# Kernel tuning notes

Hardware: AMD Instinct MI355X
Metric: run time of the kernel (lower is better)

The kernel has to match this reference:

```python
import jax, jax.numpy as jnp
import numpy as np

N, E, IN, HID, HEADS, EDGE_DIM, L = 50000, 800000, 128, 64, 4, 8, 2
NEG_SLOPE = 0.2


def setup_inputs() -> dict:
    key = jax.random.key(0)
    ks = jax.random.split(key, 12)
    s = 0.05
    return {
        "x": jax.random.normal(ks[0], (N, IN), jnp.float32),
        "edge_index": jax.random.randint(ks[1], (2, E), 0, N, jnp.int32),
        "edge_attr": jax.random.randint(ks[2], (E,), 0, 3, jnp.int32),
        "proj_w": jax.random.normal(ks[3], (IN, HID), jnp.float32) * s,
        "proj_b": jnp.zeros((HID,), jnp.float32),
        "edge_emb": jax.random.normal(ks[4], (3, EDGE_DIM), jnp.float32) * s,
        "Wl": jax.random.normal(ks[5], (L, HID, HEADS * HID), jnp.float32) * s,
        "Wr": jax.random.normal(ks[6], (L, HID, HEADS * HID), jnp.float32) * s,
        "We": jax.random.normal(ks[7], (L, EDGE_DIM, HEADS * HID), jnp.float32) * s,
        "att": jax.random.normal(ks[8], (L, HEADS, HID), jnp.float32) * s,
        "bias": jnp.zeros((L, HID), jnp.float32),
        "ln_w": jnp.ones((L, HID), jnp.float32),
        "ln_b": jnp.zeros((L, HID), jnp.float32),
    }


def _layer_norm(h, w, b, eps=1e-5):
    mu = h.mean(-1, keepdims=True)
    var = ((h - mu) ** 2).mean(-1, keepdims=True)
    return (h - mu) * jax.lax.rsqrt(var + eps) * w + b


def reference(x, edge_index, edge_attr, proj_w, proj_b, edge_emb, Wl, Wr, We, att, bias, ln_w, ln_b):
    n = x.shape[0]
    x = x @ proj_w + proj_b  # [N, HID]
    ef = edge_emb[edge_attr]  # [E, EDGE_DIM]
    # PyG GATv2Conv default: add self-loops, edge feature fill_value='mean'
    loop = jnp.arange(n, dtype=edge_index.dtype)
    src = jnp.concatenate([edge_index[0], loop])
    dst = jnp.concatenate([edge_index[1], loop])
    ef = jnp.concatenate([ef, jnp.broadcast_to(ef.mean(0), (n, ef.shape[1]))])  # [E+N, EDGE_DIM]

    for l in range(L):
        xl = (x @ Wl[l]).reshape(n, HEADS, HID)   # source transform
        xr = (x @ Wr[l]).reshape(n, HEADS, HID)   # target transform
        ee = (ef @ We[l]).reshape(-1, HEADS, HID)  # edge transform [E+N,H,C]
        m = xl[src] + xr[dst] + ee                # gather by edge -> [E+N,H,C]
        s = jnp.einsum('ehc,hc->eh', jax.nn.leaky_relu(m, NEG_SLOPE), att[l])
        # segment softmax over incoming edges of each dst node
        smax = jax.ops.segment_max(s, dst, num_segments=n)
        a = jnp.exp(s - smax[dst])
        denom = jax.ops.segment_sum(a, dst, num_segments=n)
        alpha = a / denom[dst]                    # [E+N, H]
        out = jax.ops.segment_sum(alpha[:, :, None] * xl[src], dst, num_segments=n)  # [N,H,C]
        out = out.mean(axis=1) + bias[l]          # concat=False -> head mean
        x = _layer_norm(out + x, ln_w[l], ln_b[l])
    return x
```

## Files before the change

### kernel.cpp

```cpp
#include <hip/hip_runtime.h>

constexpr int N_NODES = 50000;
constexpr int E_EDGES = 800000;
constexpr int SLOTS   = 64;
constexpr int IN_DIM  = 128;
constexpr int HID     = 64;
constexpr int HEADS   = 4;
constexpr int HH      = HEADS * HID;
constexpr int EDGE_DIM = 8;
constexpr int L_LAYERS = 2;
constexpr float NEG_SLOPE = 0.2f;
constexpr int N_STRIPS = N_NODES / 16;
constexpr int SCAT_BLKS = (E_EDGES + 255) / 256;
constexpr int PROJ_BLKS = (N_STRIPS + 15) / 16;
constexpr int CNT_BLKS  = 256;
constexpr int PAD_BLKS  = (N_NODES + 255) / 256;

typedef float floatx2 __attribute__((ext_vector_type(2)));
typedef float f32x4 __attribute__((ext_vector_type(4)));
typedef short bf16x8 __attribute__((ext_vector_type(8)));

__device__ __forceinline__ unsigned short f2bf(float f) {
    unsigned int b = __float_as_uint(f);
    unsigned int r = (b + 0x7FFFu + ((b >> 16) & 1u)) >> 16;
    return (unsigned short)r;
}
__device__ __forceinline__ float bf2f(unsigned short u) {
    return __uint_as_float(((unsigned int)u) << 16);
}
__device__ __forceinline__ float lrelu(float x) { return fmaxf(x, NEG_SLOPE * x); }

__device__ __forceinline__ unsigned char f2fp8(float v) {
    return (unsigned char)(__builtin_amdgcn_cvt_pk_fp8_f32(v, v, 0, false) & 0xFF);
}
__device__ __forceinline__ void fp8x4_to_f32(unsigned int w, float& a, float& b,
                                             float& c, float& d) {
    floatx2 lo = __builtin_amdgcn_cvt_pk_f32_fp8((int)w, false);
    floatx2 hi = __builtin_amdgcn_cvt_pk_f32_fp8((int)w, true);
    a = lo.x; b = lo.y; c = hi.x; d = hi.y;
}

__global__ void mega_kernel(const int* __restrict__ src, const int* __restrict__ dst,
                            const int* __restrict__ attr, int* __restrict__ cnt,
                            unsigned int* __restrict__ fcsr, int* __restrict__ counts,
                            const float* __restrict__ x, const float* __restrict__ w,
                            const float* __restrict__ b, float* __restrict__ x0) {
    __shared__ unsigned short wS[IN_DIM * HID];
    int bid = blockIdx.x;
    if (bid < SCAT_BLKS) {
        int e = bid * 256 + threadIdx.x;
        if (e >= E_EDGES) return;
        int d = dst[e];
        int pos = atomicAdd(&cnt[d], 1);
        if (pos < SLOTS - 1)
            fcsr[((size_t)d << 6) + pos] = (unsigned int)src[e] | ((unsigned int)attr[e] << 16);
        return;
    }
    bid -= SCAT_BLKS;
    if (bid < PROJ_BLKS) {
        for (int i = threadIdx.x; i < IN_DIM * HID; i += 256) wS[i] = f2bf(w[i]);
        __syncthreads();
        int wid = threadIdx.x >> 6, lane = threadIdx.x & 63;
        int colb = lane & 15, kb = (lane >> 4) * 8;
        bf16x8 bfr[4][4];
#pragma unroll
        for (int c = 0; c < 4; ++c)
#pragma unroll
            for (int g = 0; g < 4; ++g) {
                bf16x8 v;
#pragma unroll
                for (int j = 0; j < 8; ++j)
                    v[j] = (short)wS[(g * 32 + kb + j) * HID + c * 16 + colb];
                bfr[c][g] = v;
            }
        float bias_v[4];
#pragma unroll
        for (int c = 0; c < 4; ++c) bias_v[c] = b[c * 16 + colb];
#pragma unroll
        for (int i = 0; i < 4; ++i) {
            int s = bid * 16 + i * 4 + wid;
            if (s >= N_STRIPS) break;
            int row = s * 16 + colb;
            const float* xp = x + (size_t)row * IN_DIM + kb;
            bf16x8 af[4];
#pragma unroll
            for (int g = 0; g < 4; ++g) {
                float4 lo = *(const float4*)(xp + g * 32);
                float4 hi = *(const float4*)(xp + g * 32 + 4);
                bf16x8 v;
                v[0] = (short)f2bf(lo.x); v[1] = (short)f2bf(lo.y);
                v[2] = (short)f2bf(lo.z); v[3] = (short)f2bf(lo.w);
                v[4] = (short)f2bf(hi.x); v[5] = (short)f2bf(hi.y);
                v[6] = (short)f2bf(hi.z); v[7] = (short)f2bf(hi.w);
                af[g] = v;
            }
            int rbase = s * 16 + (lane >> 4) * 4;
#pragma unroll
            for (int c = 0; c < 4; ++c) {
                f32x4 acc = {0.f, 0.f, 0.f, 0.f};
#pragma unroll
                for (int g = 0; g < 4; ++g)
                    acc = __builtin_amdgcn_mfma_f32_16x16x32_bf16(af[g], bfr[c][g], acc, 0, 0, 0);
#pragma unroll
                for (int r = 0; r < 4; ++r)
                    x0[(size_t)(rbase + r) * HID + c * 16 + colb] = acc[r] + bias_v[c];
            }
        }
        return;
    }
    bid -= PROJ_BLKS;
    {
        int c0 = 0, c1 = 0, c2 = 0;
        for (int i = bid * 256 + threadIdx.x; i < E_EDGES; i += CNT_BLKS * 256) {
            int a = attr[i];
            c0 += (a == 0); c1 += (a == 1); c2 += (a == 2);
        }
        for (int o = 32; o; o >>= 1) {
            c0 += __shfl_down(c0, o);
            c1 += __shfl_down(c1, o);
            c2 += __shfl_down(c2, o);
        }
        if ((threadIdx.x & 63) == 0) {
            atomicAdd(&counts[0], c0);
            atomicAdd(&counts[1], c1);
            atomicAdd(&counts[2], c2);
        }
    }
}

__global__ void pad_eet_kernel(int* __restrict__ cnt, unsigned int* __restrict__ fcsr,
                               const float* __restrict__ edge_emb, const float* __restrict__ We,
                               const int* __restrict__ counts, float* __restrict__ eet) {
    if (blockIdx.x >= (unsigned)PAD_BLKS) {
        int hc = threadIdx.x;
        float inv = 1.f / (float)E_EDGES;
        for (int l = 0; l < L_LAYERS; ++l) {
            const float* We_l = We + (size_t)l * EDGE_DIM * HH;
            float* eet_l = eet + (size_t)l * 4 * HH;
            for (int t = 0; t < 3; ++t) {
                float acc = 0.f;
#pragma unroll
                for (int d = 0; d < EDGE_DIM; ++d) acc += edge_emb[t * EDGE_DIM + d] * We_l[d * HH + hc];
                eet_l[t * HH + hc] = acc;
            }
            float acc = 0.f;
#pragma unroll
            for (int d = 0; d < EDGE_DIM; ++d) {
                float md = (counts[0] * edge_emb[0 * EDGE_DIM + d] +
                            counts[1] * edge_emb[1 * EDGE_DIM + d] +
                            counts[2] * edge_emb[2 * EDGE_DIM + d]) * inv;
                acc += md * We_l[d * HH + hc];
            }
            eet_l[3 * HH + hc] = acc;
        }
        return;
    }
    int n = blockIdx.x * 256 + threadIdx.x;
    if (n >= N_NODES) return;
    int c = cnt[n];
    int tot = c + 1;
    int pad = (tot + 3) & ~3;
    unsigned int selfe = (unsigned int)n | (3u << 16);
    unsigned int* row = fcsr + ((size_t)n << 6);
    for (int p = c; p < pad; ++p) row[p] = selfe;
    cnt[n] = tot;
}

__global__ __launch_bounds__(256)
void transform_mfma_kernel(const float* __restrict__ x, const float* __restrict__ Wl,
                           const float* __restrict__ Wr, unsigned char* __restrict__ xl,
                           unsigned short* __restrict__ xr) {
    __shared__ unsigned short wS[HID * 512];
    for (int i = threadIdx.x; i < HID * 512; i += 256) {
        int k = i >> 9, c = i & 511;
        float v = (c < 256) ? Wl[k * 256 + c] : Wr[k * 256 + (c - 256)];
        wS[i] = f2bf(v);
    }
    __syncthreads();
    int wid = threadIdx.x >> 6, lane = threadIdx.x & 63;
    int colb = lane & 15, kb = (lane >> 4) * 8;
    bf16x8 bfr[8][2];
#pragma unroll
    for (int c = 0; c < 8; ++c)
#pragma unroll
        for (int g = 0; g < 2; ++g) {
            bf16x8 v;
            int col = wid * 128 + c * 16 + colb;
#pragma unroll
            for (int j = 0; j < 8; ++j)
                v[j] = (short)wS[(g * 32 + kb + j) * 512 + col];
            bfr[c][g] = v;
        }

    for (int i = 0; i < 16; ++i) {
        int s = blockIdx.x * 16 + i;
        if (s >= N_STRIPS) break;
        int row = s * 16 + colb;
        const float* xp = x + (size_t)row * HID + kb;
        bf16x8 af[2];
#pragma unroll
        for (int g = 0; g < 2; ++g) {
            float4 lo = *(const float4*)(xp + g * 32);
            float4 hi = *(const float4*)(xp + g * 32 + 4);
            bf16x8 v;
            v[0] = (short)f2bf(lo.x); v[1] = (short)f2bf(lo.y);
            v[2] = (short)f2bf(lo.z); v[3] = (short)f2bf(lo.w);
            v[4] = (short)f2bf(hi.x); v[5] = (short)f2bf(hi.y);
            v[6] = (short)f2bf(hi.z); v[7] = (short)f2bf(hi.w);
            af[g] = v;
        }
        int rbase = s * 16 + (lane >> 4) * 4;
#pragma unroll
        for (int c = 0; c < 8; ++c) {
            f32x4 acc = {0.f, 0.f, 0.f, 0.f};
            acc = __builtin_amdgcn_mfma_f32_16x16x32_bf16(af[0], bfr[c][0], acc, 0, 0, 0);
            acc = __builtin_amdgcn_mfma_f32_16x16x32_bf16(af[1], bfr[c][1], acc, 0, 0, 0);
            int col = wid * 128 + c * 16 + colb;
            if (col < 256) {
#pragma unroll
                for (int r = 0; r < 4; ++r)
                    xl[(size_t)(rbase + r) * HH + col] = f2fp8(acc[r]);
            } else {
                int c2 = col - 256;
#pragma unroll
                for (int r = 0; r < 4; ++r)
                    xr[(size_t)(rbase + r) * HH + c2] = f2bf(acc[r]);
            }
        }
    }
}

__global__ void gat_fused_kernel(const unsigned int* __restrict__ fcsr,
                                 const int* __restrict__ cnt,
                                 const unsigned char* __restrict__ xl,
                                 const unsigned short* __restrict__ xr,
                                 const float* __restrict__ eet_l, const float* __restrict__ att_l,
                                 const float* __restrict__ bias_l, const float* __restrict__ lnw,
                                 const float* __restrict__ lnb, const float* __restrict__ x_res,
                                 float* __restrict__ x_out) {
    __shared__ float4 eetS[256];
    eetS[threadIdx.x] = ((const float4*)eet_l)[threadIdx.x];
    __syncthreads();
    int n = blockIdx.x * 4 + (threadIdx.x >> 6);
    int lane = threadIdx.x & 63;
    float4 av = *(const float4*)(att_l + lane * 4);
    ushort4 xrv = *(const ushort4*)(xr + (size_t)n * HH + lane * 4);
    float xr0 = bf2f(xrv.x), xr1 = bf2f(xrv.y), xr2 = bf2f(xrv.z), xr3 = bf2f(xrv.w);
    const unsigned char* xlb = xl + lane * 4;
    int cntn = cnt[n];
    const unsigned int* cp = fcsr + ((size_t)n << 6);
    float accA0 = 0.f, accA1 = 0.f, accA2 = 0.f, accA3 = 0.f, denA = 0.f;
    float accB0 = 0.f, accB1 = 0.f, accB2 = 0.f, accB3 = 0.f, denB = 0.f;

    auto gat_round = [&](uint4 ew, unsigned int xw0, unsigned int xw1, unsigned int xw2,
                         unsigned int xw3, int rem) {
        int t0 = ew.x >> 16, t1 = ew.y >> 16, t2 = ew.z >> 16, t3 = ew.w >> 16;
        float4 ee0 = eetS[(t0 << 6) + lane];
        float4 ee1 = eetS[(t1 << 6) + lane];
        float4 ee2 = eetS[(t2 << 6) + lane];
        float4 ee3 = eetS[(t3 << 6) + lane];
        float a0, a1, a2, a3, b0, b1, b2, b3, c0, c1, c2, c3, d0, d1, d2, d3;
        fp8x4_to_f32(xw0, a0, a1, a2, a3);
        fp8x4_to_f32(xw1, b0, b1, b2, b3);
        fp8x4_to_f32(xw2, c0, c1, c2, c3);
        fp8x4_to_f32(xw3, d0, d1, d2, d3);
        float p0 = lrelu(a0 + xr0 + ee0.x) * av.x + lrelu(a1 + xr1 + ee0.y) * av.y +
                   lrelu(a2 + xr2 + ee0.z) * av.z + lrelu(a3 + xr3 + ee0.w) * av.w;
        float p1 = lrelu(b0 + xr0 + ee1.x) * av.x + lrelu(b1 + xr1 + ee1.y) * av.y +
                   lrelu(b2 + xr2 + ee1.z) * av.z + lrelu(b3 + xr3 + ee1.w) * av.w;
        float p2 = lrelu(c0 + xr0 + ee2.x) * av.x + lrelu(c1 + xr1 + ee2.y) * av.y +
                   lrelu(c2 + xr2 + ee2.z) * av.z + lrelu(c3 + xr3 + ee2.w) * av.w;
        float p3 = lrelu(d0 + xr0 + ee3.x) * av.x + lrelu(d1 + xr1 + ee3.y) * av.y +
                   lrelu(d2 + xr2 + ee3.z) * av.z + lrelu(d3 + xr3 + ee3.w) * av.w;
        p0 += __shfl_xor(p0, 1); p1 += __shfl_xor(p1, 1);
        p2 += __shfl_xor(p2, 1); p3 += __shfl_xor(p3, 1);
        p0 += __shfl_xor(p0, 2); p1 += __shfl_xor(p1, 2);
        p2 += __shfl_xor(p2, 2); p3 += __shfl_xor(p3, 2);
        p0 += __shfl_xor(p0, 4); p1 += __shfl_xor(p1, 4);
        p2 += __shfl_xor(p2, 4); p3 += __shfl_xor(p3, 4);
        p0 += __shfl_xor(p0, 8); p1 += __shfl_xor(p1, 8);
        p2 += __shfl_xor(p2, 8); p3 += __shfl_xor(p3, 8);
        float w0 = __expf(p0);
        float w1 = (rem > 1) ? __expf(p1) : 0.f;
        float w2 = (rem > 2) ? __expf(p2) : 0.f;
        float w3 = (rem > 3) ? __expf(p3) : 0.f;
        denA += w0 + w1;
        denB += w2 + w3;
        accA0 += w0 * a0 + w1 * b0;  accB0 += w2 * c0 + w3 * d0;
        accA1 += w0 * a1 + w1 * b1;  accB1 += w2 * c1 + w3 * d1;
        accA2 += w0 * a2 + w1 * b2;  accB2 += w2 * c2 + w3 * d2;
        accA3 += w0 * a3 + w1 * b3;  accB3 += w2 * c3 + w3 * d3;
    };

    int rounds = (cntn + 3) >> 2;
    uint4 ew = *(const uint4*)cp;
    unsigned int xw0 = *(const unsigned int*)(xlb + (size_t)(ew.x & 0xFFFFu) * HH);
    unsigned int xw1 = *(const unsigned int*)(xlb + (size_t)(ew.y & 0xFFFFu) * HH);
    unsigned int xw2 = *(const unsigned int*)(xlb + (size_t)(ew.z & 0xFFFFu) * HH);
    unsigned int xw3 = *(const unsigned int*)(xlb + (size_t)(ew.w & 0xFFFFu) * HH);
    for (int it = 1; it < rounds; ++it) {
        uint4 ewN = *(const uint4*)(cp + (it << 2));
        unsigned int yw0 = *(const unsigned int*)(xlb + (size_t)(ewN.x & 0xFFFFu) * HH);
        unsigned int yw1 = *(const unsigned int*)(xlb + (size_t)(ewN.y & 0xFFFFu) * HH);
        unsigned int yw2 = *(const unsigned int*)(xlb + (size_t)(ewN.z & 0xFFFFu) * HH);
        unsigned int yw3 = *(const unsigned int*)(xlb + (size_t)(ewN.w & 0xFFFFu) * HH);
        gat_round(ew, xw0, xw1, xw2, xw3, 4);
        ew = ewN; xw0 = yw0; xw1 = yw1; xw2 = yw2; xw3 = yw3;
    }
    gat_round(ew, xw0, xw1, xw2, xw3, cntn - ((rounds - 1) << 2));

    float inv = 1.f / (denA + denB);
    float r0 = (accA0 + accB0) * inv, r1 = (accA1 + accB1) * inv;
    float r2 = (accA2 + accB2) * inv, r3 = (accA3 + accB3) * inv;
    r0 += __shfl_xor(r0, 16); r1 += __shfl_xor(r1, 16);
    r2 += __shfl_xor(r2, 16); r3 += __shfl_xor(r3, 16);
    r0 += __shfl_xor(r0, 32); r1 += __shfl_xor(r1, 32);
    r2 += __shfl_xor(r2, 32); r3 += __shfl_xor(r3, 32);
    if (lane < 16) {
        float4 xc = *(const float4*)(x_res + (size_t)n * HID + lane * 4);
        float4 bb = *(const float4*)(bias_l + lane * 4);
        float h0 = 0.25f * r0 + bb.x + xc.x;
        float h1 = 0.25f * r1 + bb.y + xc.y;
        float h2 = 0.25f * r2 + bb.z + xc.z;
        float h3 = 0.25f * r3 + bb.w + xc.w;
        float sum = h0 + h1 + h2 + h3;
        sum += __shfl_xor(sum, 1); sum += __shfl_xor(sum, 2);
        sum += __shfl_xor(sum, 4); sum += __shfl_xor(sum, 8);
        float mu = sum * (1.f / 64.f);
        float d0_ = h0 - mu, d1_ = h1 - mu, d2_ = h2 - mu, d3_ = h3 - mu;
        float vs = d0_ * d0_ + d1_ * d1_ + d2_ * d2_ + d3_ * d3_;
        vs += __shfl_xor(vs, 1); vs += __shfl_xor(vs, 2);
        vs += __shfl_xor(vs, 4); vs += __shfl_xor(vs, 8);
        float rstd = rsqrtf(vs * (1.f / 64.f) + 1e-5f);
        float4 w4 = *(const float4*)(lnw + lane * 4);
        float4 b4 = *(const float4*)(lnb + lane * 4);
        float4 o;
        o.x = d0_ * rstd * w4.x + b4.x;
        o.y = d1_ * rstd * w4.y + b4.y;
        o.z = d2_ * rstd * w4.z + b4.z;
        o.w = d3_ * rstd * w4.w + b4.w;
        *(float4*)(x_out + (size_t)n * HID + lane * 4) = o;
    }
}

extern "C" void kernel_launch(void* const* d_in, const int* in_sizes, int n_in,
                              void* d_out, int out_size, void* d_ws, size_t ws_size,
                              hipStream_t stream) {
    const float* x_in     = (const float*)d_in[0];
    const int*   edge_idx = (const int*)d_in[1];
    const int*   attr     = (const int*)d_in[2];
    const float* proj_w   = (const float*)d_in[3];
    const float* proj_b   = (const float*)d_in[4];
    const float* edge_emb = (const float*)d_in[5];
    const float* Wl       = (const float*)d_in[6];
    const float* Wr       = (const float*)d_in[7];
    const float* We       = (const float*)d_in[8];
    const float* att      = (const float*)d_in[9];
    const float* bias     = (const float*)d_in[10];
    const float* ln_w     = (const float*)d_in[11];
    const float* ln_b     = (const float*)d_in[12];
    float* out = (float*)d_out;

    const int* src_idx = edge_idx;
    const int* dst_idx = edge_idx + E_EDGES;

    float* ws = (float*)d_ws;
    float* x0 = ws;
    float* x1 = x0 + (size_t)N_NODES * HID;
    unsigned char* xl_f8 = (unsigned char*)(x1 + (size_t)N_NODES * HID);
    unsigned short* xr_bf = (unsigned short*)(xl_f8 + (size_t)N_NODES * HH);
    unsigned int* fcsr = (unsigned int*)(xr_bf + (size_t)N_NODES * HH);
    int* cnt    = (int*)(fcsr + (size_t)N_NODES * SLOTS);
    int* counts = cnt + N_NODES;
    float* eet  = (float*)(counts + 4);

    hipMemsetAsync(cnt, 0, ((size_t)N_NODES + 4) * sizeof(int), stream);

    mega_kernel<<<SCAT_BLKS + PROJ_BLKS + CNT_BLKS, 256, 0, stream>>>(
        src_idx, dst_idx, attr, cnt, fcsr, counts, x_in, proj_w, proj_b, x0);
    pad_eet_kernel<<<PAD_BLKS + 1, 256, 0, stream>>>(cnt, fcsr, edge_emb, We, counts, eet);
    transform_mfma_kernel<<<PROJ_BLKS, 256, 0, stream>>>(x0, Wl, Wr, xl_f8, xr_bf);
    gat_fused_kernel<<<N_NODES / 4, 256, 0, stream>>>(fcsr, cnt, xl_f8, xr_bf, eet,
                                                      att, bias, ln_w, ln_b, x0, x1);
    transform_mfma_kernel<<<PROJ_BLKS, 256, 0, stream>>>(x1, Wl + (size_t)HID * HH,
                                                         Wr + (size_t)HID * HH, xl_f8, xr_bf);
    gat_fused_kernel<<<N_NODES / 4, 256, 0, stream>>>(fcsr, cnt, xl_f8, xr_bf,
                                                      eet + 4 * HH, att + HH, bias + HID,
                                                      ln_w + HID, ln_b + HID, x1, out);
}
```

Before: 332.0 us.

## Split each node's edge loop across two wavefronts and pad atomic counters

```diff
diff --git a/kernel.cpp b/kernel.cpp
--- a/kernel.cpp
+++ b/kernel.cpp
@@ -41,7 +41,7 @@
 }
 
 __global__ void mega_kernel(const int* __restrict__ src, const int* __restrict__ dst,
-                            const int* __restrict__ attr, int* __restrict__ cnt,
+                            const int* __restrict__ attr, int* __restrict__ cnt16,
                             unsigned int* __restrict__ fcsr, int* __restrict__ counts,
                             const float* __restrict__ x, const float* __restrict__ w,
                             const float* __restrict__ b, float* __restrict__ x0) {
@@ -51,7 +51,7 @@
         int e = bid * 256 + threadIdx.x;
         if (e >= E_EDGES) return;
         int d = dst[e];
-        int pos = atomicAdd(&cnt[d], 1);
+        int pos = atomicAdd(&cnt16[d << 4], 1);
         if (pos < SLOTS - 1)
             fcsr[((size_t)d << 6) + pos] = (unsigned int)src[e] | ((unsigned int)attr[e] << 16);
         return;
@@ -128,7 +128,7 @@
     }
 }
 
-__global__ void pad_eet_kernel(int* __restrict__ cnt, unsigned int* __restrict__ fcsr,
+__global__ void pad_eet_kernel(int* __restrict__ cnt16, unsigned int* __restrict__ fcsr,
                                const float* __restrict__ edge_emb, const float* __restrict__ We,
                                const int* __restrict__ counts, float* __restrict__ eet) {
     if (blockIdx.x >= (unsigned)PAD_BLKS) {
@@ -157,13 +157,13 @@
     }
     int n = blockIdx.x * 256 + threadIdx.x;
     if (n >= N_NODES) return;
-    int c = cnt[n];
+    int c = cnt16[n << 4];
     int tot = c + 1;
     int pad = (tot + 3) & ~3;
     unsigned int selfe = (unsigned int)n | (3u << 16);
     unsigned int* row = fcsr + ((size_t)n << 6);
     for (int p = c; p < pad; ++p) row[p] = selfe;
-    cnt[n] = tot;
+    cnt16[n << 4] = tot;
 }
 
 __global__ __launch_bounds__(256)
@@ -231,7 +231,7 @@
 }
 
 __global__ void gat_fused_kernel(const unsigned int* __restrict__ fcsr,
-                                 const int* __restrict__ cnt,
+                                 const int* __restrict__ cnt16,
                                  const unsigned char* __restrict__ xl,
                                  const unsigned short* __restrict__ xr,
                                  const float* __restrict__ eet_l, const float* __restrict__ att_l,
@@ -239,15 +239,19 @@
                                  const float* __restrict__ lnb, const float* __restrict__ x_res,
                                  float* __restrict__ x_out) {
     __shared__ float4 eetS[256];
+    __shared__ float accS[2][5][64];
     eetS[threadIdx.x] = ((const float4*)eet_l)[threadIdx.x];
     __syncthreads();
-    int n = blockIdx.x * 4 + (threadIdx.x >> 6);
+    int wid = threadIdx.x >> 6;
+    int nl = wid >> 1;
+    int sub = wid & 1;
+    int n = blockIdx.x * 2 + nl;
     int lane = threadIdx.x & 63;
     float4 av = *(const float4*)(att_l + lane * 4);
     ushort4 xrv = *(const ushort4*)(xr + (size_t)n * HH + lane * 4);
     float xr0 = bf2f(xrv.x), xr1 = bf2f(xrv.y), xr2 = bf2f(xrv.z), xr3 = bf2f(xrv.w);
     const unsigned char* xlb = xl + lane * 4;
-    int cntn = cnt[n];
+    int cntn = cnt16[n << 4];
     const unsigned int* cp = fcsr + ((size_t)n << 6);
     float accA0 = 0.f, accA1 = 0.f, accA2 = 0.f, accA3 = 0.f, denA = 0.f;
     float accB0 = 0.f, accB1 = 0.f, accB2 = 0.f, accB3 = 0.f, denB = 0.f;
@@ -293,25 +297,42 @@
     };
 
     int rounds = (cntn + 3) >> 2;
-    uint4 ew = *(const uint4*)cp;
-    unsigned int xw0 = *(const unsigned int*)(xlb + (size_t)(ew.x & 0xFFFFu) * HH);
-    unsigned int xw1 = *(const unsigned int*)(xlb + (size_t)(ew.y & 0xFFFFu) * HH);
-    unsigned int xw2 = *(const unsigned int*)(xlb + (size_t)(ew.z & 0xFFFFu) * HH);
-    unsigned int xw3 = *(const unsigned int*)(xlb + (size_t)(ew.w & 0xFFFFu) * HH);
-    for (int it = 1; it < rounds; ++it) {
-        uint4 ewN = *(const uint4*)(cp + (it << 2));
-        unsigned int yw0 = *(const unsigned int*)(xlb + (size_t)(ewN.x & 0xFFFFu) * HH);
-        unsigned int yw1 = *(const unsigned int*)(xlb + (size_t)(ewN.y & 0xFFFFu) * HH);
-        unsigned int yw2 = *(const unsigned int*)(xlb + (size_t)(ewN.z & 0xFFFFu) * HH);
-        unsigned int yw3 = *(const unsigned int*)(xlb + (size_t)(ewN.w & 0xFFFFu) * HH);
-        gat_round(ew, xw0, xw1, xw2, xw3, 4);
-        ew = ewN; xw0 = yw0; xw1 = yw1; xw2 = yw2; xw3 = yw3;
-    }
-    gat_round(ew, xw0, xw1, xw2, xw3, cntn - ((rounds - 1) << 2));
-
-    float inv = 1.f / (denA + denB);
-    float r0 = (accA0 + accB0) * inv, r1 = (accA1 + accB1) * inv;
-    float r2 = (accA2 + accB2) * inv, r3 = (accA3 + accB3) * inv;
+    if (sub < rounds) {
+        int cur = sub;
+        uint4 ew = *(const uint4*)(cp + (cur << 2));
+        unsigned int xw0 = *(const unsigned int*)(xlb + (size_t)(ew.x & 0xFFFFu) * HH);
+        unsigned int xw1 = *(const unsigned int*)(xlb + (size_t)(ew.y & 0xFFFFu) * HH);
+        unsigned int xw2 = *(const unsigned int*)(xlb + (size_t)(ew.z & 0xFFFFu) * HH);
+        unsigned int xw3 = *(const unsigned int*)(xlb + (size_t)(ew.w & 0xFFFFu) * HH);
+        for (int nx = cur + 2; nx < rounds; nx += 2) {
+            uint4 ewN = *(const uint4*)(cp + (nx << 2));
+            unsigned int yw0 = *(const unsigned int*)(xlb + (size_t)(ewN.x & 0xFFFFu) * HH);
+            unsigned int yw1 = *(const unsigned int*)(xlb + (size_t)(ewN.y & 0xFFFFu) * HH);
+            unsigned int yw2 = *(const unsigned int*)(xlb + (size_t)(ewN.z & 0xFFFFu) * HH);
+            unsigned int yw3 = *(const unsigned int*)(xlb + (size_t)(ewN.w & 0xFFFFu) * HH);
+            gat_round(ew, xw0, xw1, xw2, xw3, 4);
+            ew = ewN; xw0 = yw0; xw1 = yw1; xw2 = yw2; xw3 = yw3;
+            cur = nx;
+        }
+        gat_round(ew, xw0, xw1, xw2, xw3, cntn - (cur << 2));
+    }
+
+    float a0 = accA0 + accB0, a1 = accA1 + accB1;
+    float a2 = accA2 + accB2, a3 = accA3 + accB3;
+    float den = denA + denB;
+    if (sub == 1) {
+        accS[nl][0][lane] = a0; accS[nl][1][lane] = a1;
+        accS[nl][2][lane] = a2; accS[nl][3][lane] = a3;
+        accS[nl][4][lane] = den;
+    }
+    __syncthreads();
+    if (sub == 1) return;
+    a0 += accS[nl][0][lane]; a1 += accS[nl][1][lane];
+    a2 += accS[nl][2][lane]; a3 += accS[nl][3][lane];
+    den += accS[nl][4][lane];
+
+    float inv = 1.f / den;
+    float r0 = a0 * inv, r1 = a1 * inv, r2 = a2 * inv, r3 = a3 * inv;
     r0 += __shfl_xor(r0, 16); r1 += __shfl_xor(r1, 16);
     r2 += __shfl_xor(r2, 16); r3 += __shfl_xor(r3, 16);
     r0 += __shfl_xor(r0, 32); r1 += __shfl_xor(r1, 32);
@@ -370,21 +391,21 @@
     unsigned char* xl_f8 = (unsigned char*)(x1 + (size_t)N_NODES * HID);
     unsigned short* xr_bf = (unsigned short*)(xl_f8 + (size_t)N_NODES * HH);
     unsigned int* fcsr = (unsigned int*)(xr_bf + (size_t)N_NODES * HH);
-    int* cnt    = (int*)(fcsr + (size_t)N_NODES * SLOTS);
-    int* counts = cnt + N_NODES;
+    int* cnt16  = (int*)(fcsr + (size_t)N_NODES * SLOTS);
+    int* counts = cnt16 + (size_t)N_NODES * 16;
     float* eet  = (float*)(counts + 4);
 
-    hipMemsetAsync(cnt, 0, ((size_t)N_NODES + 4) * sizeof(int), stream);
+    hipMemsetAsync(cnt16, 0, ((size_t)N_NODES * 16 + 4) * sizeof(int), stream);
 
     mega_kernel<<<SCAT_BLKS + PROJ_BLKS + CNT_BLKS, 256, 0, stream>>>(
-        src_idx, dst_idx, attr, cnt, fcsr, counts, x_in, proj_w, proj_b, x0);
-    pad_eet_kernel<<<PAD_BLKS + 1, 256, 0, stream>>>(cnt, fcsr, edge_emb, We, counts, eet);
+        src_idx, dst_idx, attr, cnt16, fcsr, counts, x_in, proj_w, proj_b, x0);
+    pad_eet_kernel<<<PAD_BLKS + 1, 256, 0, stream>>>(cnt16, fcsr, edge_emb, We, counts, eet);
     transform_mfma_kernel<<<PROJ_BLKS, 256, 0, stream>>>(x0, Wl, Wr, xl_f8, xr_bf);
-    gat_fused_kernel<<<N_NODES / 4, 256, 0, stream>>>(fcsr, cnt, xl_f8, xr_bf, eet,
+    gat_fused_kernel<<<N_NODES / 2, 256, 0, stream>>>(fcsr, cnt16, xl_f8, xr_bf, eet,
                                                       att, bias, ln_w, ln_b, x0, x1);
     transform_mfma_kernel<<<PROJ_BLKS, 256, 0, stream>>>(x1, Wl + (size_t)HID * HH,
                                                          Wr + (size_t)HID * HH, xl_f8, xr_bf);
-    gat_fused_kernel<<<N_NODES / 4, 256, 0, stream>>>(fcsr, cnt, xl_f8, xr_bf,
+    gat_fused_kernel<<<N_NODES / 2, 256, 0, stream>>>(fcsr, cnt16, xl_f8, xr_bf,
                                                       eet + 4 * HH, att + HH, bias + HID,
                                                       ln_w + HID, ln_b + HID, x1, out);
 }
```

Measured after the change: 386.1 us. +16.3%, slower.

## Sort nodes by degree bucket so GAT waves process similar-length rows

Applied to the files above, without the earlier changes.

```diff
diff --git a/kernel.cpp b/kernel.cpp
--- a/kernel.cpp
+++ b/kernel.cpp
@@ -15,6 +15,7 @@
 constexpr int PROJ_BLKS = (N_STRIPS + 15) / 16;
 constexpr int CNT_BLKS  = 256;
 constexpr int PAD_BLKS  = (N_NODES + 255) / 256;
+constexpr int NBINS     = 32;
 
 typedef float floatx2 __attribute__((ext_vector_type(2)));
 typedef float f32x4 __attribute__((ext_vector_type(4)));
@@ -129,6 +130,7 @@
 }
 
 __global__ void pad_eet_kernel(int* __restrict__ cnt, unsigned int* __restrict__ fcsr,
+                               int* __restrict__ bins16,
                                const float* __restrict__ edge_emb, const float* __restrict__ We,
                                const int* __restrict__ counts, float* __restrict__ eet) {
     if (blockIdx.x >= (unsigned)PAD_BLKS) {
@@ -155,15 +157,55 @@
         }
         return;
     }
+    __shared__ int h[NBINS];
+    if (threadIdx.x < NBINS) h[threadIdx.x] = 0;
+    __syncthreads();
     int n = blockIdx.x * 256 + threadIdx.x;
-    if (n >= N_NODES) return;
-    int c = cnt[n];
-    int tot = c + 1;
-    int pad = (tot + 3) & ~3;
-    unsigned int selfe = (unsigned int)n | (3u << 16);
-    unsigned int* row = fcsr + ((size_t)n << 6);
-    for (int p = c; p < pad; ++p) row[p] = selfe;
-    cnt[n] = tot;
+    if (n < N_NODES) {
+        int c = cnt[n];
+        if (c > SLOTS - 1) c = SLOTS - 1;
+        int tot = c + 1;
+        int pad = (tot + 3) & ~3;
+        unsigned int selfe = (unsigned int)n | (3u << 16);
+        unsigned int* row = fcsr + ((size_t)n << 6);
+        for (int p = c; p < pad; ++p) row[p] = selfe;
+        cnt[n] = tot;
+        atomicAdd(&h[pad >> 2], 1);
+    }
+    __syncthreads();
+    if (threadIdx.x < NBINS && h[threadIdx.x])
+        atomicAdd(&bins16[threadIdx.x << 4], h[threadIdx.x]);
+}
+
+__global__ void scan_bins_kernel(const int* __restrict__ bins16, int* __restrict__ cur16) {
+    int b = threadIdx.x;
+    if (b < NBINS) {
+        int base = 0;
+        for (int j = NBINS - 1; j > b; --j) base += bins16[j << 4];
+        cur16[b << 4] = base;
+    }
+}
+
+__global__ void order_kernel(const int* __restrict__ cnt, int* __restrict__ cur16,
+                             int* __restrict__ order) {
+    __shared__ int h[NBINS], base[NBINS], loc[NBINS];
+    if (threadIdx.x < NBINS) { h[threadIdx.x] = 0; loc[threadIdx.x] = 0; }
+    __syncthreads();
+    int n = blockIdx.x * 256 + threadIdx.x;
+    bool valid = n < N_NODES;
+    int rb = 0;
+    if (valid) {
+        rb = (cnt[n] + 3) >> 2;
+        atomicAdd(&h[rb], 1);
+    }
+    __syncthreads();
+    if (threadIdx.x < NBINS && h[threadIdx.x])
+        base[threadIdx.x] = atomicAdd(&cur16[threadIdx.x << 4], h[threadIdx.x]);
+    __syncthreads();
+    if (valid) {
+        int r = atomicAdd(&loc[rb], 1);
+        order[base[rb] + r] = n;
+    }
 }
 
 __global__ __launch_bounds__(256)
@@ -232,6 +274,7 @@
 
 __global__ void gat_fused_kernel(const unsigned int* __restrict__ fcsr,
                                  const int* __restrict__ cnt,
+                                 const int* __restrict__ order,
                                  const unsigned char* __restrict__ xl,
                                  const unsigned short* __restrict__ xr,
                                  const float* __restrict__ eet_l, const float* __restrict__ att_l,
@@ -241,7 +284,7 @@
     __shared__ float4 eetS[256];
     eetS[threadIdx.x] = ((const float4*)eet_l)[threadIdx.x];
     __syncthreads();
-    int n = blockIdx.x * 4 + (threadIdx.x >> 6);
+    int n = order[blockIdx.x * 4 + (threadIdx.x >> 6)];
     int lane = threadIdx.x & 63;
     float4 av = *(const float4*)(att_l + lane * 4);
     ushort4 xrv = *(const ushort4*)(xr + (size_t)n * HH + lane * 4);
@@ -372,19 +415,25 @@
     unsigned int* fcsr = (unsigned int*)(xr_bf + (size_t)N_NODES * HH);
     int* cnt    = (int*)(fcsr + (size_t)N_NODES * SLOTS);
     int* counts = cnt + N_NODES;
-    float* eet  = (float*)(counts + 4);
-
-    hipMemsetAsync(cnt, 0, ((size_t)N_NODES + 4) * sizeof(int), stream);
+    int* bins16 = counts + 4;
+    int* cur16  = bins16 + NBINS * 16;
+    int* order  = cur16 + NBINS * 16;
+    float* eet  = (float*)(order + N_NODES);
+
+    hipMemsetAsync(cnt, 0, ((size_t)N_NODES + 4 + NBINS * 16) * sizeof(int), stream);
 
     mega_kernel<<<SCAT_BLKS + PROJ_BLKS + CNT_BLKS, 256, 0, stream>>>(
         src_idx, dst_idx, attr, cnt, fcsr, counts, x_in, proj_w, proj_b, x0);
-    pad_eet_kernel<<<PAD_BLKS + 1, 256, 0, stream>>>(cnt, fcsr, edge_emb, We, counts, eet);
+    pad_eet_kernel<<<PAD_BLKS + 1, 256, 0, stream>>>(cnt, fcsr, bins16,
+                                                     edge_emb, We, counts, eet);
+    scan_bins_kernel<<<1, 64, 0, stream>>>(bins16, cur16);
+    order_kernel<<<PAD_BLKS, 256, 0, stream>>>(cnt, cur16, order);
     transform_mfma_kernel<<<PROJ_BLKS, 256, 0, stream>>>(x0, Wl, Wr, xl_f8, xr_bf);
-    gat_fused_kernel<<<N_NODES / 4, 256, 0, stream>>>(fcsr, cnt, xl_f8, xr_bf, eet,
+    gat_fused_kernel<<<N_NODES / 4, 256, 0, stream>>>(fcsr, cnt, order, xl_f8, xr_bf, eet,
                                                       att, bias, ln_w, ln_b, x0, x1);
     transform_mfma_kernel<<<PROJ_BLKS, 256, 0, stream>>>(x1, Wl + (size_t)HID * HH,
                                                          Wr + (size_t)HID * HH, xl_f8, xr_bf);
-    gat_fused_kernel<<<N_NODES / 4, 256, 0, stream>>>(fcsr, cnt, xl_f8, xr_bf,
+    gat_fused_kernel<<<N_NODES / 4, 256, 0, stream>>>(fcsr, cnt, order, xl_f8, xr_bf,
                                                       eet + 4 * HH, att + HH, bias + HID,
                                                       ln_w + HID, ln_b + HID, x1, out);
 }
```

Result: no change. 334.7 us (+0.8%).
